# Kernel optimization log

Measured on AMD Instinct MI355X. Metric: run time of the kernel, lower is better.

The kernel has to match this reference:

```python
import jax, jax.numpy as jnp
import numpy as np

B, L, E, H = 4, 2048, 1024, 16
HD = E // H  # 64
ROPE_BASE = 10000.0


def setup_inputs() -> dict:
    key = jax.random.key(0)
    ks = jax.random.split(key, 4)
    x = jax.random.normal(ks[0], (B, L, E), dtype=jnp.float32)
    Wqkv = jax.random.normal(ks[1], (3 * E, E), dtype=jnp.float32) * (E ** -0.5)
    bqkv = jnp.zeros((3 * E,), dtype=jnp.float32)
    Wout = jax.random.normal(ks[2], (E, E), dtype=jnp.float32) * (E ** -0.5)
    bout = jnp.zeros((E,), dtype=jnp.float32)
    # RoPE tables: (1, 1, L, HD/2)
    half = HD // 2
    inv_freq = 1.0 / (ROPE_BASE ** (jnp.arange(half, dtype=jnp.float32) / half))
    t = jnp.arange(L, dtype=jnp.float32)
    freqs = t[:, None] * inv_freq[None, :]  # (L, half)
    cos = jnp.cos(freqs)[None, None]
    sin = jnp.sin(freqs)[None, None]
    return {"x": x, "cos": cos, "sin": sin, "Wqkv": Wqkv, "bqkv": bqkv,
            "Wout": Wout, "bout": bout}


def _apply_rope(q, k, cos, sin):
    half = q.shape[-1] // 2
    q1, q2 = q[..., :half], q[..., half:]
    k1, k2 = k[..., :half], k[..., half:]
    q_rot = jnp.concatenate([q1 * cos - q2 * sin, q1 * sin + q2 * cos], axis=-1)
    k_rot = jnp.concatenate([k1 * cos - k2 * sin, k1 * sin + k2 * cos], axis=-1)
    return q_rot, k_rot


def reference(x, cos, sin, Wqkv, bqkv, Wout, bout):
    b, l, e = x.shape
    qkv = x @ Wqkv.T + bqkv  # (B, L, 3E)
    q, k, v = jnp.split(qkv, 3, axis=-1)
    # (B, H, L, HD)
    q = q.reshape(b, l, H, HD).transpose(0, 2, 1, 3)
    k = k.reshape(b, l, H, HD).transpose(0, 2, 1, 3)
    v = v.reshape(b, l, H, HD).transpose(0, 2, 1, 3)
    q, k = _apply_rope(q, k, cos, sin)
    scale = 1.0 / jnp.sqrt(jnp.asarray(HD, dtype=x.dtype))
    scores = jnp.einsum('bhqd,bhkd->bhqk', q, k) * scale
    attn = jax.nn.softmax(scores, axis=-1)
    out = jnp.einsum('bhqk,bhkd->bhqd', attn, v)  # (B, H, L, HD)
    out = out.transpose(0, 2, 1, 3).reshape(b, l, e)
    out = out @ Wout.T + bout
    return out
```

## Files before the change

### kernel.cpp

```cpp
#include <hip/hip_runtime.h>
#include <math.h>

#define B 4
#define L 2048
#define E 1024
#define H 16
#define HD 64
#define MROWS (B*L)
#define E3 (3*E)
#define LSTR 72

using bf16x8   = __attribute__((ext_vector_type(8))) short;
using f16x8    = __attribute__((ext_vector_type(8))) _Float16;
using floatx4  = __attribute__((ext_vector_type(4))) float;
using floatx16 = __attribute__((ext_vector_type(16))) float;

__device__ inline ushort f2bf(float x) {
    uint u = __float_as_uint(x);
    u += 0x7FFF + ((u >> 16) & 1);
    return (ushort)(u >> 16);
}
__device__ inline float bf2f(ushort h) { return __uint_as_float(((uint)h) << 16); }
__device__ inline ushort f2h(float x) { _Float16 h = (_Float16)x; return *(ushort*)&h; }

#if __has_builtin(__builtin_amdgcn_exp2f)
#define EXP2F(x) __builtin_amdgcn_exp2f(x)
#else
#define EXP2F(x) exp2f(x)
#endif

__device__ inline void async16(const void* g, void* l) {
    __builtin_amdgcn_global_load_lds(
        (const __attribute__((address_space(1))) uint*)g,
        (__attribute__((address_space(3))) uint*)l, 16, 0, 0);
}

__device__ inline uint pack_rtz(float odd, float even) {
    return __builtin_amdgcn_perm(__float_as_uint(odd), __float_as_uint(even), 0x07060302u);
}

#define N1Q ((size_t)MROWS * E / 4)
#define N2Q ((size_t)E3 * E / 4)
#define N3Q ((size_t)E * E / 4)
__global__ __launch_bounds__(256) void cvt_all(
        const float* __restrict__ x, const float* __restrict__ wq,
        const float* __restrict__ wo, ushort* __restrict__ x16,
        ushort* __restrict__ wq16, ushort* __restrict__ wo16)
{
    size_t i = (size_t)blockIdx.x * 256 + threadIdx.x;
    const float* src; ushort* dst; size_t j;
    if (i < N1Q)                  { src = x;  dst = x16;  j = i; }
    else if (i < N1Q + N2Q)       { src = wq; dst = wq16; j = i - N1Q; }
    else                          { src = wo; dst = wo16; j = i - N1Q - N2Q; }
    float4 v = ((const float4*)src)[j];
    ushort4 o;
    o.x = f2h(v.x); o.y = f2h(v.y); o.z = f2h(v.z); o.w = f2h(v.w);
    ((ushort4*)dst)[j] = o;
}

template<int MODE>
__global__ __launch_bounds__(256) void gemm_f16(
        const ushort* __restrict__ A16, const ushort* __restrict__ B16,
        const float* __restrict__ bias, float* __restrict__ Cf,
        ushort* __restrict__ qh, ushort* __restrict__ kh, ushort* __restrict__ vT,
        const float* __restrict__ cosT, const float* __restrict__ sinT,
        int Ndim, int Kdim)
{
    __shared__ ushort lds[8192];

    const int tid = threadIdx.x;
    const int w = tid >> 6, lane = tid & 63;
    const int g = lane >> 4, c = lane & 15;
    const int m0 = blockIdx.y * 128, n0 = blockIdx.x * 128;
    const int wm = w & 1, wn = w >> 1;

    const int rl0 = lane >> 2;
    const int jsw = (lane & 3) ^ ((lane >> 3) & 3);
    const ushort* gbase = (w < 2) ? A16 + (size_t)(m0 + 64 * (w & 1)) * Kdim
                                  : B16 + (size_t)(n0 + 64 * (w & 1)) * Kdim;
    const ushort* lanesrc = gbase + (size_t)rl0 * Kdim + jsw * 8;
    ushort* ldst = &lds[(w >> 1) * 4096 + (w & 1) * 2048];

    floatx4 acc[4][4];
#pragma unroll
    for (int a = 0; a < 4; ++a)
#pragma unroll
        for (int bq = 0; bq < 4; ++bq) acc[a][bq] = (floatx4){0.f, 0.f, 0.f, 0.f};

    const int swz  = (g ^ ((c >> 1) & 3)) * 8;
    const int arow = wm * 2048 + c * 32;
    const int brow = 4096 + wn * 2048 + c * 32;

    for (int k0 = 0; k0 < Kdim; k0 += 32) {
        __syncthreads();
#pragma unroll
        for (int p = 0; p < 4; ++p)
            async16(lanesrc + (size_t)p * 16 * Kdim + k0, ldst + p * 512);
        asm volatile("s_waitcnt vmcnt(0)" ::: "memory");
        __syncthreads();

        f16x8 af[4], bf[4];
#pragma unroll
        for (int t = 0; t < 4; ++t) {
            af[t] = *(const f16x8*)&lds[arow + t * 512 + swz];
            bf[t] = *(const f16x8*)&lds[brow + t * 512 + swz];
        }
#pragma unroll
        for (int mt = 0; mt < 4; ++mt)
#pragma unroll
            for (int nt = 0; nt < 4; ++nt)
                acc[mt][nt] = __builtin_amdgcn_mfma_f32_16x16x32_f16(af[mt], bf[nt], acc[mt][nt], 0, 0, 0);
    }

    const int colbase = n0 + wn * 64;
#pragma unroll
    for (int mt = 0; mt < 4; ++mt) {
        const int rowb = m0 + wm * 64 + mt * 16 + g * 4;
        if constexpr (MODE == 2) {
#pragma unroll
            for (int i = 0; i < 4; ++i) {
                const int row = rowb + i;
#pragma unroll
                for (int nt = 0; nt < 4; ++nt) {
                    const int col = colbase + nt * 16 + c;
                    Cf[(size_t)row * Ndim + col] = acc[mt][nt][i] + bias[col];
                }
            }
        } else {
            const int sec = colbase >> 10;
            const int hg  = (colbase & 1023) >> 6;
#pragma unroll
            for (int i = 0; i < 4; ++i) {
                const int row = rowb + i;
                const int bb = row >> 11;
                const int l  = row & (L - 1);
                if (sec < 2) {
                    ushort* dst = (sec == 0 ? qh : kh) + ((size_t)(bb * H + hg) * L + l) * HD;
                    const float qs = (sec == 0) ? 0.18033688f : 1.0f;
#pragma unroll
                    for (int nt = 0; nt < 2; ++nt) {
                        const int d = nt * 16 + c;
                        float v1 = acc[mt][nt][i]     + bias[colbase + d];
                        float v2 = acc[mt][nt + 2][i] + bias[colbase + d + 32];
                        float cs = cosT[l * 32 + d], sn = sinT[l * 32 + d];
                        dst[d]      = f2bf((v1 * cs - v2 * sn) * qs);
                        dst[d + 32] = f2bf((v1 * sn + v2 * cs) * qs);
                    }
                } else {
#pragma unroll
                    for (int nt = 0; nt < 4; ++nt) {
                        const int d = nt * 16 + c;
                        float v = acc[mt][nt][i] + bias[colbase + d];
                        vT[((size_t)(bb * H + hg) * HD + d) * L + l] = f2bf(v);
                    }
                }
            }
        }
    }
}

__global__ __launch_bounds__(256, 3) void flash_mfma3(
        const ushort* __restrict__ qh, const ushort* __restrict__ kh,
        const ushort* __restrict__ vT, ushort* __restrict__ attn16)
{
    __shared__ ushort Ks[2][64 * LSTR];
    __shared__ ushort Vt[2][64 * LSTR];

    const int tid  = threadIdx.x;
    const int w    = tid >> 6;
    const int lane = tid & 63;
    const int h    = lane >> 5;
    const int n    = lane & 31;
    const int b    = blockIdx.x >> 4;
    const int hd   = blockIdx.x & 15;
    const int q0   = blockIdx.y * 128;

    const ushort* khead = kh + (size_t)(b * H + hd) * L * HD;
    const ushort* vhead = vT + (size_t)(b * H + hd) * HD * L;

    const int q = q0 + 32 * w + n;
    const ushort* qptr = qh + ((size_t)(b * H + hd) * L + q) * HD + 8 * h;
    bf16x8 aq[4];
#pragma unroll
    for (int kd = 0; kd < 4; ++kd)
        aq[kd] = *(const bf16x8*)(qptr + 16 * kd);

    const int sr = tid >> 3, sj8 = (tid & 7) * 8;
    const ushort* ks0 = khead + (size_t)sr * HD + sj8;
    const ushort* vs0 = vhead + (size_t)sr * L + sj8;
    ushort* kw0 = &Ks[0][sr * LSTR + sj8];
    ushort* kw1 = &Ks[0][(sr + 32) * LSTR + sj8];
    ushort* vw0 = &Vt[0][sr * LSTR + sj8];
    ushort* vw1 = &Vt[0][(sr + 32) * LSTR + sj8];
    const int bufoff = 64 * LSTR;

    uint4 kr0, kr1, vr0, vr1;
    kr0 = *(const uint4*)(ks0);
    kr1 = *(const uint4*)(ks0 + 32 * HD);
    vr0 = *(const uint4*)(vs0);
    vr1 = *(const uint4*)(vs0 + (size_t)32 * L);
    *(uint4*)kw0 = kr0; *(uint4*)kw1 = kr1;
    *(uint4*)vw0 = vr0; *(uint4*)vw1 = vr1;
    kr0 = *(const uint4*)(ks0 + (size_t)64 * HD);
    kr1 = *(const uint4*)(ks0 + (size_t)96 * HD);
    vr0 = *(const uint4*)(vs0 + 64);
    vr1 = *(const uint4*)(vs0 + (size_t)32 * L + 64);
    __syncthreads();

    float l_i = 0.f;
    floatx16 o[2];
    o[0] = (floatx16)(0.f);
    o[1] = (floatx16)(0.f);

    const int NIT = L / 64;
    for (int it = 0; it < NIT; ++it) {
        const int p = it & 1;
        const ushort* KsC = &Ks[0][p * bufoff];
        const ushort* VtC = &Vt[0][p * bufoff];

        if (it + 1 < NIT) {
            const int po = (p ^ 1) * bufoff;
            *(uint4*)(kw0 + po) = kr0; *(uint4*)(kw1 + po) = kr1;
            *(uint4*)(vw0 + po) = vr0; *(uint4*)(vw1 + po) = vr1;
        }
        if (it + 2 < NIT) {
            const size_t t = (size_t)(it + 2) * 64;
            kr0 = *(const uint4*)(ks0 + t * HD);
            kr1 = *(const uint4*)(ks0 + (t + 32) * HD);
            vr0 = *(const uint4*)(vs0 + t);
            vr1 = *(const uint4*)(vs0 + (size_t)32 * L + t);
        }

#pragma unroll
        for (int js = 0; js < 2; ++js) {
            floatx16 s = (floatx16)(-16.0f);
#pragma unroll
            for (int kd = 0; kd < 4; ++kd) {
                bf16x8 kf = *(const bf16x8*)&KsC[(32 * js + n) * LSTR + 16 * kd + 8 * h];
                s = __builtin_amdgcn_mfma_f32_32x32x16_bf16(kf, aq[kd], s, 0, 0, 0);
            }

            float pv[16]; float rs = 0.f;
#pragma unroll
            for (int r = 0; r < 16; ++r) { pv[r] = EXP2F(s[r]); rs += pv[r]; }
            l_i += rs;

            uint pku[4][2];
#pragma unroll
            for (int rr = 0; rr < 4; ++rr) {
                pku[rr][0] = pack_rtz(pv[4 * rr + 1], pv[4 * rr + 0]);
                pku[rr][1] = pack_rtz(pv[4 * rr + 3], pv[4 * rr + 2]);
            }

            uint bp_u[2][4];
#pragma unroll
            for (int f = 0; f < 2; ++f) {
                const int rA = 2 * f, rB = 2 * f + 1;
                uint mm0 = h ? pku[rB][0] : pku[rA][0];
                uint mm1 = h ? pku[rB][1] : pku[rA][1];
                uint mp0 = h ? pku[rA][0] : pku[rB][0];
                uint mp1 = h ? pku[rA][1] : pku[rB][1];
                uint g0 = (uint)__shfl_xor((int)mp0, 32, 64);
                uint g1 = (uint)__shfl_xor((int)mp1, 32, 64);
                bp_u[f][0] = h ? g0 : mm0;
                bp_u[f][1] = h ? g1 : mm1;
                bp_u[f][2] = h ? mm0 : g0;
                bp_u[f][3] = h ? mm1 : g1;
            }

#pragma unroll
            for (int f = 0; f < 2; ++f) {
                bf16x8 bp = *(const bf16x8*)&bp_u[f][0];
#pragma unroll
                for (int nt = 0; nt < 2; ++nt) {
                    bf16x8 vf = *(const bf16x8*)&VtC[(32 * nt + n) * LSTR + 32 * js + 16 * f + 8 * h];
                    o[nt] = __builtin_amdgcn_mfma_f32_32x32x16_bf16(vf, bp, o[nt], 0, 0, 0);
                }
            }
        }
        __syncthreads();
    }

    const float l_tot = l_i + __shfl_xor(l_i, 32, 64);
    const float inv = 1.f / l_tot;
    const size_t rowbase = ((size_t)(b * L + q)) * E + hd * HD;
#pragma unroll
    for (int nt = 0; nt < 2; ++nt)
#pragma unroll
        for (int rr = 0; rr < 4; ++rr) {
            const int d0 = 32 * nt + 8 * rr + 4 * h;
            ushort h0 = f2h(o[nt][4 * rr + 0] * inv);
            ushort h1 = f2h(o[nt][4 * rr + 1] * inv);
            ushort h2 = f2h(o[nt][4 * rr + 2] * inv);
            ushort h3 = f2h(o[nt][4 * rr + 3] * inv);
            uint2 hw;
            hw.x = (uint)h0 | ((uint)h1 << 16);
            hw.y = (uint)h2 | ((uint)h3 << 16);
            *(uint2*)&attn16[rowbase + d0] = hw;
        }
}

extern "C" void kernel_launch(void* const* d_in, const int* in_sizes, int n_in,
                              void* d_out, int out_size, void* d_ws, size_t ws_size,
                              hipStream_t stream) {
    const float* x    = (const float*)d_in[0];
    const float* cosT = (const float*)d_in[1];
    const float* sinT = (const float*)d_in[2];
    const float* Wqkv = (const float*)d_in[3];
    const float* bqkv = (const float*)d_in[4];
    const float* Wout = (const float*)d_in[5];
    const float* bout = (const float*)d_in[6];
    float* out = (float*)d_out;

    const size_t NX = (size_t)MROWS * E;
    ushort* us   = (ushort*)d_ws;
    ushort* qh   = us;
    ushort* kh   = us + NX;
    ushort* vTp  = us + 2 * NX;
    ushort* x16  = us + 3 * NX;
    ushort* at16 = us + 4 * NX;
    ushort* wq16 = us + 5 * NX;
    ushort* wo16 = wq16 + (size_t)E3 * E;

    const int cvt_blocks = (int)((N1Q + N2Q + N3Q + 255) / 256);
    cvt_all<<<cvt_blocks, 256, 0, stream>>>(x, Wqkv, Wout, x16, wq16, wo16);

    gemm_f16<1><<<dim3(E3 / 128, MROWS / 128), 256, 0, stream>>>(
        x16, wq16, bqkv, nullptr, qh, kh, vTp, cosT, sinT, E3, E);

    flash_mfma3<<<dim3(B * H, L / 128), 256, 0, stream>>>(qh, kh, vTp, at16);

    gemm_f16<2><<<dim3(E / 128, MROWS / 128), 256, 0, stream>>>(
        at16, wo16, bout, out, nullptr, nullptr, nullptr, nullptr, nullptr, E, E);
}
```

Before: 341.4 us.

## Swizzle Q/K/V global layout and stream K/V tiles via async loads

```diff
diff --git a/kernel.cpp b/kernel.cpp
--- a/kernel.cpp
+++ b/kernel.cpp
@@ -8,7 +8,6 @@
 #define HD 64
 #define MROWS (B*L)
 #define E3 (3*E)
-#define LSTR 72
 
 using bf16x8   = __attribute__((ext_vector_type(8))) short;
 using f16x8    = __attribute__((ext_vector_type(8))) _Float16;
@@ -136,22 +135,28 @@
                 const int l  = row & (L - 1);
                 if (sec < 2) {
                     ushort* dst = (sec == 0 ? qh : kh) + ((size_t)(bb * H + hg) * L + l) * HD;
+                    const int sw = l & 7;
                     const float qs = (sec == 0) ? 0.18033688f : 1.0f;
 #pragma unroll
                     for (int nt = 0; nt < 2; ++nt) {
-                        const int d = nt * 16 + c;
+                        const int d  = nt * 16 + c;
+                        const int d2 = d + 32;
                         float v1 = acc[mt][nt][i]     + bias[colbase + d];
-                        float v2 = acc[mt][nt + 2][i] + bias[colbase + d + 32];
+                        float v2 = acc[mt][nt + 2][i] + bias[colbase + d2];
                         float cs = cosT[l * 32 + d], sn = sinT[l * 32 + d];
-                        dst[d]      = f2bf((v1 * cs - v2 * sn) * qs);
-                        dst[d + 32] = f2bf((v1 * sn + v2 * cs) * qs);
+                        dst[(((d  >> 3) ^ sw) << 3) | (d  & 7)] = f2bf((v1 * cs - v2 * sn) * qs);
+                        dst[(((d2 >> 3) ^ sw) << 3) | (d2 & 7)] = f2bf((v1 * sn + v2 * cs) * qs);
                     }
                 } else {
+                    const int lp = (l & ~12) | ((l & 4) << 1) | ((l & 8) >> 1);
+                    const int intile = ((((lp >> 3) & 7)) << 3);
 #pragma unroll
                     for (int nt = 0; nt < 4; ++nt) {
                         const int d = nt * 16 + c;
                         float v = acc[mt][nt][i] + bias[colbase + d];
-                        vT[((size_t)(bb * H + hg) * HD + d) * L + l] = f2bf(v);
+                        size_t idx = ((size_t)(bb * H + hg) * HD + d) * L
+                                   + (l & ~63) + (intile ^ ((d & 7) << 3)) + (lp & 7);
+                        vT[idx] = f2bf(v);
                     }
                 }
             }
@@ -159,12 +164,12 @@
     }
 }
 
-__global__ __launch_bounds__(256, 3) void flash_mfma3(
+__global__ __launch_bounds__(256, 4) void flash_mfma4(
         const ushort* __restrict__ qh, const ushort* __restrict__ kh,
         const ushort* __restrict__ vT, ushort* __restrict__ attn16)
 {
-    __shared__ ushort Ks[2][64 * LSTR];
-    __shared__ ushort Vt[2][64 * LSTR];
+    __shared__ ushort Ks[2][4096];
+    __shared__ ushort Vt[2][4096];
 
     const int tid  = threadIdx.x;
     const int w    = tid >> 6;
@@ -179,106 +184,91 @@
     const ushort* vhead = vT + (size_t)(b * H + hd) * HD * L;
 
     const int q = q0 + 32 * w + n;
-    const ushort* qptr = qh + ((size_t)(b * H + hd) * L + q) * HD + 8 * h;
+    const ushort* qrow = qh + ((size_t)(b * H + hd) * L + q) * HD;
     bf16x8 aq[4];
 #pragma unroll
     for (int kd = 0; kd < 4; ++kd)
-        aq[kd] = *(const bf16x8*)(qptr + 16 * kd);
-
-    const int sr = tid >> 3, sj8 = (tid & 7) * 8;
-    const ushort* ks0 = khead + (size_t)sr * HD + sj8;
-    const ushort* vs0 = vhead + (size_t)sr * L + sj8;
-    ushort* kw0 = &Ks[0][sr * LSTR + sj8];
-    ushort* kw1 = &Ks[0][(sr + 32) * LSTR + sj8];
-    ushort* vw0 = &Vt[0][sr * LSTR + sj8];
-    ushort* vw1 = &Vt[0][(sr + 32) * LSTR + sj8];
-    const int bufoff = 64 * LSTR;
-
-    uint4 kr0, kr1, vr0, vr1;
-    kr0 = *(const uint4*)(ks0);
-    kr1 = *(const uint4*)(ks0 + 32 * HD);
-    vr0 = *(const uint4*)(vs0);
-    vr1 = *(const uint4*)(vs0 + (size_t)32 * L);
-    *(uint4*)kw0 = kr0; *(uint4*)kw1 = kr1;
-    *(uint4*)vw0 = vr0; *(uint4*)vw1 = vr1;
-    kr0 = *(const uint4*)(ks0 + (size_t)64 * HD);
-    kr1 = *(const uint4*)(ks0 + (size_t)96 * HD);
-    vr0 = *(const uint4*)(vs0 + 64);
-    vr1 = *(const uint4*)(vs0 + (size_t)32 * L + 64);
-    __syncthreads();
+        aq[kd] = *(const bf16x8*)&qrow[((2 * kd + h) ^ (q & 7)) << 3];
+
+    const int wk = w & 1;
+    const ushort* ksrc = khead + (size_t)(32 * wk) * 64 + lane * 8;
+    const ushort* vsrc = vhead + (size_t)(32 * wk + (lane >> 3)) * L + (lane & 7) * 8;
+
+    const int NIT = L / 64;
+    if (w < 2) {
+#pragma unroll
+        for (int p = 0; p < 4; ++p)
+            async16(ksrc + p * 512, &Ks[0][32 * wk * 64 + p * 512]);
+    } else {
+#pragma unroll
+        for (int p = 0; p < 4; ++p)
+            async16(vsrc + (size_t)p * 8 * L, &Vt[0][32 * wk * 64 + p * 512]);
+    }
 
     float l_i = 0.f;
     floatx16 o[2];
     o[0] = (floatx16)(0.f);
     o[1] = (floatx16)(0.f);
 
-    const int NIT = L / 64;
     for (int it = 0; it < NIT; ++it) {
         const int p = it & 1;
-        const ushort* KsC = &Ks[0][p * bufoff];
-        const ushort* VtC = &Vt[0][p * bufoff];
+        __syncthreads();
 
         if (it + 1 < NIT) {
-            const int po = (p ^ 1) * bufoff;
-            *(uint4*)(kw0 + po) = kr0; *(uint4*)(kw1 + po) = kr1;
-            *(uint4*)(vw0 + po) = vr0; *(uint4*)(vw1 + po) = vr1;
-        }
-        if (it + 2 < NIT) {
-            const size_t t = (size_t)(it + 2) * 64;
-            kr0 = *(const uint4*)(ks0 + t * HD);
-            kr1 = *(const uint4*)(ks0 + (t + 32) * HD);
-            vr0 = *(const uint4*)(vs0 + t);
-            vr1 = *(const uint4*)(vs0 + (size_t)32 * L + t);
-        }
+            if (w < 2) {
+                const ushort* s = ksrc + (size_t)(it + 1) * 4096;
+#pragma unroll
+                for (int pp = 0; pp < 4; ++pp)
+                    async16(s + pp * 512, &Ks[p ^ 1][32 * wk * 64 + pp * 512]);
+            } else {
+                const ushort* s = vsrc + (size_t)(it + 1) * 64;
+#pragma unroll
+                for (int pp = 0; pp < 4; ++pp)
+                    async16(s + (size_t)pp * 8 * L, &Vt[p ^ 1][32 * wk * 64 + pp * 512]);
+            }
+        }
+
+        const ushort* KsC = Ks[p];
+        const ushort* VtC = Vt[p];
 
 #pragma unroll
         for (int js = 0; js < 2; ++js) {
             floatx16 s = (floatx16)(-16.0f);
 #pragma unroll
             for (int kd = 0; kd < 4; ++kd) {
-                bf16x8 kf = *(const bf16x8*)&KsC[(32 * js + n) * LSTR + 16 * kd + 8 * h];
+                bf16x8 kf = *(const bf16x8*)&KsC[(32 * js + n) * 64 + (((2 * kd + h) ^ (n & 7)) << 3)];
                 s = __builtin_amdgcn_mfma_f32_32x32x16_bf16(kf, aq[kd], s, 0, 0, 0);
             }
 
-            float pv[16]; float rs = 0.f;
-#pragma unroll
-            for (int r = 0; r < 16; ++r) { pv[r] = EXP2F(s[r]); rs += pv[r]; }
+            float pv[16];
+            float rs = 0.f;
+#pragma unroll
+            for (int rr = 0; rr < 4; ++rr) {
+                float p0 = EXP2F(s[4 * rr + 0]);
+                float p1 = EXP2F(s[4 * rr + 1]);
+                float p2 = EXP2F(s[4 * rr + 2]);
+                float p3 = EXP2F(s[4 * rr + 3]);
+                pv[4 * rr + 0] = p0; pv[4 * rr + 1] = p1;
+                pv[4 * rr + 2] = p2; pv[4 * rr + 3] = p3;
+                rs += (p0 + p1) + (p2 + p3);
+            }
             l_i += rs;
 
-            uint pku[4][2];
-#pragma unroll
-            for (int rr = 0; rr < 4; ++rr) {
-                pku[rr][0] = pack_rtz(pv[4 * rr + 1], pv[4 * rr + 0]);
-                pku[rr][1] = pack_rtz(pv[4 * rr + 3], pv[4 * rr + 2]);
-            }
-
-            uint bp_u[2][4];
 #pragma unroll
             for (int f = 0; f < 2; ++f) {
-                const int rA = 2 * f, rB = 2 * f + 1;
-                uint mm0 = h ? pku[rB][0] : pku[rA][0];
-                uint mm1 = h ? pku[rB][1] : pku[rA][1];
-                uint mp0 = h ? pku[rA][0] : pku[rB][0];
-                uint mp1 = h ? pku[rA][1] : pku[rB][1];
-                uint g0 = (uint)__shfl_xor((int)mp0, 32, 64);
-                uint g1 = (uint)__shfl_xor((int)mp1, 32, 64);
-                bp_u[f][0] = h ? g0 : mm0;
-                bp_u[f][1] = h ? g1 : mm1;
-                bp_u[f][2] = h ? mm0 : g0;
-                bp_u[f][3] = h ? mm1 : g1;
-            }
-
-#pragma unroll
-            for (int f = 0; f < 2; ++f) {
-                bf16x8 bp = *(const bf16x8*)&bp_u[f][0];
+                uint bu[4];
+                bu[0] = pack_rtz(pv[8 * f + 1], pv[8 * f + 0]);
+                bu[1] = pack_rtz(pv[8 * f + 3], pv[8 * f + 2]);
+                bu[2] = pack_rtz(pv[8 * f + 5], pv[8 * f + 4]);
+                bu[3] = pack_rtz(pv[8 * f + 7], pv[8 * f + 6]);
+                bf16x8 bp = *(const bf16x8*)&bu[0];
 #pragma unroll
                 for (int nt = 0; nt < 2; ++nt) {
-                    bf16x8 vf = *(const bf16x8*)&VtC[(32 * nt + n) * LSTR + 32 * js + 16 * f + 8 * h];
+                    bf16x8 vf = *(const bf16x8*)&VtC[(32 * nt + n) * 64 + (((4 * js + 2 * f + h) ^ (n & 7)) << 3)];
                     o[nt] = __builtin_amdgcn_mfma_f32_32x32x16_bf16(vf, bp, o[nt], 0, 0, 0);
                 }
             }
         }
-        __syncthreads();
     }
 
     const float l_tot = l_i + __shfl_xor(l_i, 32, 64);
@@ -328,7 +318,7 @@
     gemm_f16<1><<<dim3(E3 / 128, MROWS / 128), 256, 0, stream>>>(
         x16, wq16, bqkv, nullptr, qh, kh, vTp, cosT, sinT, E3, E);
 
-    flash_mfma3<<<dim3(B * H, L / 128), 256, 0, stream>>>(qh, kh, vTp, at16);
+    flash_mfma4<<<dim3(B * H, L / 128), 256, 0, stream>>>(qh, kh, vTp, at16);
 
     gemm_f16<2><<<dim3(E / 128, MROWS / 128), 256, 0, stream>>>(
         at16, wo16, bout, out, nullptr, nullptr, nullptr, nullptr, nullptr, E, E);
```

Result: faster. 287.9 us (-15.6%).
